# Kernel tuning notes

Measured on AMD Instinct MI355X. Metric: run time of the kernel, lower is better.

Reference implementation:

```python
import jax, jax.numpy as jnp
import numpy as np

BASE_K = 256
MAX_K = 512


def setup_inputs() -> dict:
    key = jax.random.key(0)
    kq, ks, kw, kb = jax.random.split(key, 4)
    B, S, D = 4, 4096, 1024
    Q = jax.random.normal(kq, (B, S, D), dtype=jnp.float32)
    scores = jax.random.normal(ks, (B, S, S), dtype=jnp.float32)
    # importance_net = nn.Linear(dim, 1): weight [1, dim], bias [1]
    bound = 1.0 / np.sqrt(D)
    W = jax.random.uniform(kw, (D,), dtype=jnp.float32, minval=-bound, maxval=bound)
    b = jax.random.uniform(kb, (1,), dtype=jnp.float32, minval=-bound, maxval=bound)
    return {"Q": Q, "scores": scores, "W": W, "b": b}


def reference(Q, scores, W, b):
    # importance gate: sigmoid(Linear(Q)) -> [B, S]
    importance = jax.nn.sigmoid(jnp.einsum("bsd,d->bs", Q, W) + b[0])
    # k per query; torch .long() truncates toward zero (values positive -> floor)
    k_per_query = (BASE_K + (MAX_K - BASE_K) * importance).astype(jnp.int32)
    # torch code does `indices, values = torch.topk(...)`, so the returned
    # 'indices' are actually the top-k VALUES. Reproduce faithfully.
    topk_values, _ = jax.lax.top_k(scores, MAX_K)  # [B, S, MAX_K]
    return topk_values, k_per_query
```

## Files before the change

### kernel.cpp

```cpp
#include <hip/hip_runtime.h>

#define SDIM 4096
#define DDIM 1024
#define NROWS 16384
#define KOUT 512
#define CAP 1024

__device__ __forceinline__ unsigned f2key(float f) {
    unsigned u = __float_as_uint(f);
    return (u & 0x80000000u) ? ~u : (u | 0x80000000u);
}
__device__ __forceinline__ float key2f(unsigned k) {
    unsigned u = (k & 0x80000000u) ? (k ^ 0x80000000u) : ~k;
    return __uint_as_float(u);
}
__device__ __forceinline__ unsigned lt_popc(unsigned long long m) {
    return __builtin_amdgcn_mbcnt_hi((unsigned)(m >> 32),
           __builtin_amdgcn_mbcnt_lo((unsigned)(m & 0xFFFFFFFFull), 0u));
}
__device__ __forceinline__ void wave_lds_fence() {
    asm volatile("s_waitcnt lgkmcnt(0)" ::: "memory");
}

__global__ __launch_bounds__(256, 1) void fused_kernel(
    const float* __restrict__ scores, const float* __restrict__ Q,
    const float* __restrict__ W, const float* __restrict__ bias,
    float* __restrict__ out_topk, float* __restrict__ out_k) {

    __shared__ unsigned sel[4][KOUT];
    __shared__ unsigned cbuf[4][CAP];

    const int tid  = threadIdx.x;
    const int lane = tid & 63;
    const int wid  = tid >> 6;
    const int row  = blockIdx.x * 4 + wid;

    {
        const float4* q4 = (const float4*)(Q + (size_t)row * DDIM);
        const float4* w4 = (const float4*)W;
        float g = 0.f;
#pragma unroll
        for (int i = 0; i < 4; ++i) {
            float4 a = q4[lane + 64 * i];
            float4 b = w4[lane + 64 * i];
            g += a.x * b.x + a.y * b.y + a.z * b.z + a.w * b.w;
        }
#pragma unroll
        for (int off = 32; off; off >>= 1) g += __shfl_down(g, off, 64);
        if (lane == 0) {
            float x   = g + bias[0];
            float imp = 1.0f / (1.0f + expf(-x));
            out_k[row] = (float)(int)(256.0f + 256.0f * imp);
        }
    }

    unsigned key[64];
    {
        const float4* src = (const float4*)(scores + (size_t)row * SDIM);
#pragma unroll
        for (int i = 0; i < 16; ++i) {
            float4 v = src[lane + 64 * i];
            key[4 * i + 0] = f2key(v.x);
            key[4 * i + 1] = f2key(v.y);
            key[4 * i + 2] = f2key(v.z);
            key[4 * i + 3] = f2key(v.w);
        }
    }

    unsigned prefix = 0;
    unsigned cnt    = 4096;
    int      bnext  = -1;
    bool     trig   = false;
#pragma unroll 1
    for (int b = 31; b >= 0; --b) {
        const unsigned candk = prefix | (1u << b);
        unsigned total = 0;
#pragma unroll
        for (int i = 0; i < 64; ++i)
            total += (unsigned)__popcll(__ballot(key[i] >= candk));
        if (total >= (unsigned)KOUT) {
            prefix = candk;
            cnt    = total;
            if (cnt <= (unsigned)CAP) { bnext = b - 1; trig = true; break; }
        }
    }

    unsigned T;
    unsigned mtot = 0;

    if (trig) {
        {
            unsigned c = 0;
#pragma unroll
            for (int i = 0; i < 64; ++i) {
                bool p = key[i] >= prefix;
                unsigned long long m = __ballot(p);
                if (p) cbuf[wid][c + lt_popc(m)] = key[i];
                c += (unsigned)__popcll(m);
            }
        }
        wave_lds_fence();

        unsigned ck[16];
#pragma unroll
        for (int j = 0; j < 16; ++j) {
            unsigned idx = (unsigned)lane + 64u * (unsigned)j;
            unsigned v = cbuf[wid][idx];
            ck[j] = (idx < cnt) ? v : 0u;
        }

        if (cnt > (unsigned)KOUT) {
#pragma unroll 1
            for (int b = bnext; b >= 0; --b) {
                const unsigned candk = prefix | (1u << b);
                unsigned total = 0;
#pragma unroll
                for (int j = 0; j < 16; ++j)
                    total += (unsigned)__popcll(__ballot(ck[j] >= candk));
                if (total >= (unsigned)KOUT) {
                    prefix = candk;
                    if (total == (unsigned)KOUT) break;
                }
            }
        }

        unsigned tmin = 0xFFFFFFFFu;
#pragma unroll
        for (int j = 0; j < 16; ++j) {
            unsigned t = (ck[j] >= prefix) ? ck[j] : 0xFFFFFFFFu;
            tmin = t < tmin ? t : tmin;
        }
#pragma unroll
        for (int off = 32; off; off >>= 1) {
            unsigned o = __shfl_xor(tmin, off, 64);
            tmin = o < tmin ? o : tmin;
        }
        T = tmin;

#pragma unroll
        for (int j = 0; j < 16; ++j) {
            bool p = ck[j] > T;
            unsigned long long m = __ballot(p);
            if (p) sel[wid][mtot + lt_popc(m)] = ck[j];
            mtot += (unsigned)__popcll(m);
        }
    } else {
        T = prefix;
#pragma unroll
        for (int i = 0; i < 64; ++i) {
            bool p = key[i] > T;
            unsigned long long m = __ballot(p);
            if (p) sel[wid][mtot + lt_popc(m)] = key[i];
            mtot += (unsigned)__popcll(m);
        }
    }

    wave_lds_fence();

    unsigned x[8];
#pragma unroll
    for (int r = 0; r < 8; ++r) {
        unsigned idx = 8 * (unsigned)lane + r;
        unsigned v = sel[wid][idx];
        x[r] = (idx < mtot) ? v : T;
    }

#pragma unroll
    for (int kk = 2; kk <= 512; kk <<= 1) {
#pragma unroll
        for (int j = kk >> 1; j >= 8; j >>= 1) {
            bool km = ((((8 * lane) & kk) == 0) == (((8 * lane) & j) == 0));
#pragma unroll
            for (int r = 0; r < 8; ++r) {
                unsigned p  = __shfl_xor(x[r], j >> 3, 64);
                unsigned mx = x[r] > p ? x[r] : p;
                unsigned mn = x[r] > p ? p : x[r];
                x[r] = km ? mx : mn;
            }
        }
#pragma unroll
        for (int j = (kk >> 1) < 4 ? (kk >> 1) : 4; j >= 1; j >>= 1) {
#pragma unroll
            for (int r = 0; r < 8; ++r) {
                if ((r & j) == 0) {
                    int rp = r | j;
                    unsigned a = x[r], b = x[rp];
                    bool d = (((8 * lane + r) & kk) == 0);
                    unsigned hi = a > b ? a : b;
                    unsigned lo = a > b ? b : a;
                    x[r]  = d ? hi : lo;
                    x[rp] = d ? lo : hi;
                }
            }
        }
    }

    float4* dst = (float4*)(out_topk + (size_t)row * KOUT);
    dst[2 * lane + 0] = make_float4(key2f(x[0]), key2f(x[1]), key2f(x[2]), key2f(x[3]));
    dst[2 * lane + 1] = make_float4(key2f(x[4]), key2f(x[5]), key2f(x[6]), key2f(x[7]));
}

extern "C" void kernel_launch(void* const* d_in, const int* in_sizes, int n_in,
                              void* d_out, int out_size, void* d_ws, size_t ws_size,
                              hipStream_t stream) {
    const float* Q      = (const float*)d_in[0];
    const float* scores = (const float*)d_in[1];
    const float* W      = (const float*)d_in[2];
    const float* b      = (const float*)d_in[3];
    float* out_topk = (float*)d_out;
    float* out_k    = (float*)d_out + (size_t)NROWS * KOUT;

    fused_kernel<<<NROWS / 4, 256, 0, stream>>>(scores, Q, W, b, out_topk, out_k);
}
```

Before: 457.1 us.

## Seed top-k radix select with fixed threshold guess and shrink candidate buffer

Each row's keys are first compacted against a fixed threshold key that corresponds to a value of 1.0. When the surviving count falls between 512 and 768, the expensive bit-by-bit radix search over all 4096 keys is skipped, and the radix refinement runs only on the small candidate set of 12 registers per lane. If the count falls outside that range, the original full radix search runs as a fallback. The separate selection buffer is merged into the candidate buffer and its capacity drops to 768, which cuts LDS use. The fast path depends on the score distribution: it pays off for standard-normal-like rows and otherwise only adds one extra compaction pass.

```diff
diff --git a/kernel.cpp b/kernel.cpp
--- a/kernel.cpp
+++ b/kernel.cpp
@@ -4,7 +4,9 @@
 #define DDIM 1024
 #define NROWS 16384
 #define KOUT 512
-#define CAP 1024
+#define CAP 768
+
+#define T0GUESS 0xBF800000u
 
 __device__ __forceinline__ unsigned f2key(float f) {
     unsigned u = __float_as_uint(f);
@@ -27,7 +29,6 @@
     const float* __restrict__ W, const float* __restrict__ bias,
     float* __restrict__ out_topk, float* __restrict__ out_k) {
 
-    __shared__ unsigned sel[4][KOUT];
     __shared__ unsigned cbuf[4][CAP];
 
     const int tid  = threadIdx.x;
@@ -67,67 +68,93 @@
         }
     }
 
-    unsigned prefix = 0;
-    unsigned cnt    = 4096;
-    int      bnext  = -1;
-    bool     trig   = false;
-#pragma unroll 1
-    for (int b = 31; b >= 0; --b) {
-        const unsigned candk = prefix | (1u << b);
-        unsigned total = 0;
-#pragma unroll
-        for (int i = 0; i < 64; ++i)
-            total += (unsigned)__popcll(__ballot(key[i] >= candk));
-        if (total >= (unsigned)KOUT) {
-            prefix = candk;
-            cnt    = total;
-            if (cnt <= (unsigned)CAP) { bnext = b - 1; trig = true; break; }
+    unsigned cnt = 0;
+    {
+#pragma unroll
+        for (int i = 0; i < 64; ++i) {
+            bool p = key[i] >= T0GUESS;
+            unsigned long long m = __ballot(p);
+            unsigned a = cnt + lt_popc(m);
+            if (p && a < CAP) cbuf[wid][a] = key[i];
+            cnt += (unsigned)__popcll(m);
         }
     }
 
     unsigned T;
     unsigned mtot = 0;
-
-    if (trig) {
-        {
+    bool have = (cnt >= (unsigned)KOUT) && (cnt <= (unsigned)CAP);
+
+    if (!have) {
+        unsigned prefix = 0;
+        unsigned tot    = SDIM;
+        bool     trig   = false;
+#pragma unroll 1
+        for (int b = 31; b >= 0; --b) {
+            const unsigned candk = prefix | (1u << b);
+            unsigned total = 0;
+#pragma unroll
+            for (int i = 0; i < 64; ++i)
+                total += (unsigned)__popcll(__ballot(key[i] >= candk));
+            if (total >= (unsigned)KOUT) {
+                prefix = candk;
+                tot    = total;
+                if (total <= (unsigned)CAP) { trig = true; break; }
+            }
+        }
+        if (trig) {
+            cnt  = tot;
+            have = true;
             unsigned c = 0;
 #pragma unroll
             for (int i = 0; i < 64; ++i) {
                 bool p = key[i] >= prefix;
                 unsigned long long m = __ballot(p);
-                if (p) cbuf[wid][c + lt_popc(m)] = key[i];
+                unsigned a = c + lt_popc(m);
+                if (p && a < CAP) cbuf[wid][a] = key[i];
                 c += (unsigned)__popcll(m);
             }
-        }
+        } else {
+            T = prefix;
+#pragma unroll
+            for (int i = 0; i < 64; ++i) {
+                bool p = key[i] > T;
+                unsigned long long m = __ballot(p);
+                if (p) cbuf[wid][mtot + lt_popc(m)] = key[i];
+                mtot += (unsigned)__popcll(m);
+            }
+        }
+    }
+
+    if (have) {
         wave_lds_fence();
 
-        unsigned ck[16];
-#pragma unroll
-        for (int j = 0; j < 16; ++j) {
+        unsigned ck[12];
+#pragma unroll
+        for (int j = 0; j < 12; ++j) {
             unsigned idx = (unsigned)lane + 64u * (unsigned)j;
             unsigned v = cbuf[wid][idx];
             ck[j] = (idx < cnt) ? v : 0u;
         }
 
+        unsigned pfx = 0;
         if (cnt > (unsigned)KOUT) {
 #pragma unroll 1
-            for (int b = bnext; b >= 0; --b) {
-                const unsigned candk = prefix | (1u << b);
+            for (int b = 31; b >= 0; --b) {
+                const unsigned candk = pfx | (1u << b);
                 unsigned total = 0;
 #pragma unroll
-                for (int j = 0; j < 16; ++j)
+                for (int j = 0; j < 12; ++j)
                     total += (unsigned)__popcll(__ballot(ck[j] >= candk));
                 if (total >= (unsigned)KOUT) {
-                    prefix = candk;
+                    pfx = candk;
                     if (total == (unsigned)KOUT) break;
                 }
             }
         }
-
         unsigned tmin = 0xFFFFFFFFu;
 #pragma unroll
-        for (int j = 0; j < 16; ++j) {
-            unsigned t = (ck[j] >= prefix) ? ck[j] : 0xFFFFFFFFu;
+        for (int j = 0; j < 12; ++j) {
+            unsigned t = (ck[j] >= pfx) ? ck[j] : 0xFFFFFFFFu;
             tmin = t < tmin ? t : tmin;
         }
 #pragma unroll
@@ -138,19 +165,10 @@
         T = tmin;
 
 #pragma unroll
-        for (int j = 0; j < 16; ++j) {
+        for (int j = 0; j < 12; ++j) {
             bool p = ck[j] > T;
             unsigned long long m = __ballot(p);
-            if (p) sel[wid][mtot + lt_popc(m)] = ck[j];
-            mtot += (unsigned)__popcll(m);
-        }
-    } else {
-        T = prefix;
-#pragma unroll
-        for (int i = 0; i < 64; ++i) {
-            bool p = key[i] > T;
-            unsigned long long m = __ballot(p);
-            if (p) sel[wid][mtot + lt_popc(m)] = key[i];
+            if (p) cbuf[wid][mtot + lt_popc(m)] = ck[j];
             mtot += (unsigned)__popcll(m);
         }
     }
@@ -161,7 +179,7 @@
 #pragma unroll
     for (int r = 0; r < 8; ++r) {
         unsigned idx = 8 * (unsigned)lane + r;
-        unsigned v = sel[wid][idx];
+        unsigned v = cbuf[wid][idx];
         x[r] = (idx < mtot) ? v : T;
     }
 
```

New measurement: 425.7 us. 6.9% less time.
